# Kernel optimization log

Hardware: AMD Instinct MI355X
Metric: run time of the kernel (lower is better)

## Reference

```python
import jax, jax.numpy as jnp
import numpy as np


def setup_inputs() -> dict:
    key = jax.random.key(0)
    kq, kk, kv = jax.random.split(key, 3)
    B, S, H, D = 1, 4096, 16, 64
    q = jax.random.normal(kq, (B, S, H, D), dtype=jnp.float32)
    k = jax.random.normal(kk, (B, S, H, D), dtype=jnp.float32)
    v = jax.random.normal(kv, (B, S, H, D), dtype=jnp.float32)
    return {"q": q, "k": k, "v": v, "causal": 1}


def reference(q, k, v, causal):
    B, S, H, D = q.shape
    scale = D ** (-0.5)
    # scores: [B, H, S_q, S_k]
    scores = jnp.einsum("bqhd,bkhd->bhqk", q, k) * scale
    if causal:
        mask = jnp.triu(jnp.ones((S, S), dtype=bool), k=1)  # True above diagonal
        scores = jnp.where(mask, -jnp.inf, scores)
    attn = jax.nn.softmax(scores, axis=-1)
    out = jnp.einsum("bhqk,bkhd->bqhd", attn, v)
    return out
```

## Files before the change

kernel.cpp:

```cpp
#include <hip/hip_runtime.h>
#include <stdint.h>

#define S_LEN 4096
#define NH    16
#define HD    64
#define RSTR  (NH * HD)
#define LRSTR 18

typedef __attribute__((ext_vector_type(8))) __bf16 bf16x8;
typedef __attribute__((ext_vector_type(4))) short short4v;
typedef __attribute__((ext_vector_type(4))) float floatx4;

union BF8 { unsigned short u[8]; unsigned d[4]; uint4 q; bf16x8 v; };
union BF4 { unsigned short u[4]; unsigned d[2]; short4v s; };

__device__ __forceinline__ unsigned pkbf(float a, float b) {
    unsigned ua = __builtin_bit_cast(unsigned, a) + 0x8000u;
    unsigned ub = __builtin_bit_cast(unsigned, b) + 0x8000u;
    return __builtin_amdgcn_perm(ub, ua, 0x07060302u);
}

__device__ __forceinline__ floatx4 mfma16(short4v a, short4v b, floatx4 c) {
#if __has_builtin(__builtin_amdgcn_mfma_f32_16x16x16bf16_1k)
    return __builtin_amdgcn_mfma_f32_16x16x16bf16_1k(a, b, c, 0, 0, 0);
#else
    floatx4 d;
    asm volatile("v_mfma_f32_16x16x16_bf16 %0, %1, %2, %3\n\ts_nop 7\n\ts_nop 7"
                 : "=v"(d) : "v"(a), "v"(b), "v"(c));
    return d;
#endif
}

__device__ __forceinline__ void gl16(const void* g, void* l) {
#if __has_builtin(__builtin_amdgcn_global_load_lds)
    __builtin_amdgcn_global_load_lds((const __attribute__((address_space(1))) unsigned int*)g,
                                     (__attribute__((address_space(3))) unsigned int*)l, 16, 0, 0);
#else
    *(uint4*)l = *(const uint4*)g;
#endif
}

__global__ __launch_bounds__(256)
void pp_kv(const float* __restrict__ K, const float* __restrict__ V,
           unsigned short* __restrict__ Kz, unsigned short* __restrict__ Vz) {
    const int bid = blockIdx.x;
    const int h   = bid & 15;
    const int tau = bid >> 4;
    const int tid = threadIdx.x;
    {
        const int r = tid >> 2, gg = tid & 3;
        const float* kp = K + ((size_t)(64 * tau + r) * NH + h) * HD + 16 * gg;
        const float4 a = *reinterpret_cast<const float4*>(kp);
        const float4 b = *reinterpret_cast<const float4*>(kp + 4);
        const float4 c = *reinterpret_cast<const float4*>(kp + 8);
        const float4 d = *reinterpret_cast<const float4*>(kp + 12);
        uint4 f0, f1;
        f0.x = pkbf(a.x, a.y); f0.y = pkbf(a.z, a.w);
        f0.z = pkbf(b.x, b.y); f0.w = pkbf(b.z, b.w);
        f1.x = pkbf(c.x, c.y); f1.y = pkbf(c.z, c.w);
        f1.z = pkbf(d.x, d.y); f1.w = pkbf(d.z, d.w);
        unsigned short* out = Kz + ((size_t)(h * 64 + tau)) * 4096 + r * 64;
        *reinterpret_cast<uint4*>(out + (((2 * gg)     ^ (r & 7)) * 8)) = f0;
        *reinterpret_cast<uint4*>(out + (((2 * gg + 1) ^ (r & 7)) * 8)) = f1;
    }
    {
        const int dr = tid & 63, kg = tid >> 6;
        const float* vp = V + ((size_t)(64 * tau + 16 * kg) * NH + h) * HD + dr;
        float x[16];
        #pragma unroll
        for (int j = 0; j < 16; ++j) x[j] = vp[(size_t)j * RSTR];
        uint4 g0, g1;
        g0.x = pkbf(x[0],  x[1]);  g0.y = pkbf(x[2],  x[3]);
        g0.z = pkbf(x[4],  x[5]);  g0.w = pkbf(x[6],  x[7]);
        g1.x = pkbf(x[8],  x[9]);  g1.y = pkbf(x[10], x[11]);
        g1.z = pkbf(x[12], x[13]); g1.w = pkbf(x[14], x[15]);
        unsigned short* out = Vz + ((size_t)(h * 64 + tau)) * 4096 + dr * 64;
        *reinterpret_cast<uint4*>(out + (((2 * kg)     ^ (dr & 7)) * 8)) = g0;
        *reinterpret_cast<uint4*>(out + (((2 * kg + 1) ^ (dr & 7)) * 8)) = g1;
    }
}

__global__ __launch_bounds__(256, 4)
void fa_main(const float* __restrict__ Q, const unsigned short* __restrict__ Kz,
             const unsigned short* __restrict__ Vz, const int* __restrict__ causal_p,
             float* __restrict__ O) {
    __shared__ __align__(16) unsigned char smem[40960];
    unsigned short* Klds = (unsigned short*)smem;
    unsigned short* Vlds = (unsigned short*)(smem + 16384);
    unsigned short* Qlds = (unsigned short*)(smem + 32768);
    float* Lsum = (float*)smem;
    float* Lred = (float*)(smem + 16384);

    const int bid = blockIdx.x;
    const int h   = bid & 15;
    const int s   = bid >> 4;
    const int jj  = s & 15;
    const int kk  = s >> 4;
    int x;
    if (kk == 0) x = jj; else if (kk == 1) x = 31 - jj;
    else if (kk == 2) x = 32 + jj; else x = 63 - jj;
    const int q0 = x * 64;

    const int tid = threadIdx.x;
    const int wv  = tid >> 6;
    const int ln  = tid & 63;
    const int c16 = ln & 15;
    const int qd  = ln >> 4;
    const int causal = causal_p[0];

    const float SC = 0.18033688011112042f;

    {
        const int r = tid >> 2, gg = tid & 3;
        const float* qp = Q + ((size_t)(q0 + r) * NH + h) * HD + 16 * gg;
        const float4 a = *reinterpret_cast<const float4*>(qp);
        const float4 b = *reinterpret_cast<const float4*>(qp + 4);
        const float4 c = *reinterpret_cast<const float4*>(qp + 8);
        const float4 d = *reinterpret_cast<const float4*>(qp + 12);
        uint4 f0, f1;
        f0.x = pkbf(a.x * SC, a.y * SC); f0.y = pkbf(a.z * SC, a.w * SC);
        f0.z = pkbf(b.x * SC, b.y * SC); f0.w = pkbf(b.z * SC, b.w * SC);
        f1.x = pkbf(c.x * SC, c.y * SC); f1.y = pkbf(c.z * SC, c.w * SC);
        f1.z = pkbf(d.x * SC, d.y * SC); f1.w = pkbf(d.z * SC, d.w * SC);
        unsigned short* out = Qlds + r * 64;
        *reinterpret_cast<uint4*>(out + (((2 * gg)     ^ (r & 7)) * 8)) = f0;
        *reinterpret_cast<uint4*>(out + (((2 * gg + 1) ^ (r & 7)) * 8)) = f1;
    }

    const char* kg = (const char*)Kz + (size_t)h * 64 * 8192 + wv * 2048 + ln * 16;
    const char* vg = (const char*)Vz + (size_t)h * 64 * 8192 + wv * 2048 + ln * 16;
    char* kl = (char*)smem + wv * 2048 + ln * 16;
    char* vl = (char*)smem + 16384 + wv * 2048 + ln * 16;

#define GLDS_TILE(IT, BUF) do {                                  \
    const char* ks_ = kg + (size_t)(IT) * 8192;                  \
    const char* vs_ = vg + (size_t)(IT) * 8192;                  \
    char* kd_ = kl + (BUF) * 8192;                               \
    char* vd_ = vl + (BUF) * 8192;                               \
    gl16(ks_, kd_); gl16(ks_ + 1024, kd_ + 1024);                \
    gl16(vs_, vd_); gl16(vs_ + 1024, vd_ + 1024);                \
} while (0)

    const int nIter = causal ? (x + 1) : (S_LEN / 64);

    floatx4 acc[4][4];
    #pragma unroll
    for (int m = 0; m < 4; ++m)
        #pragma unroll
        for (int t = 0; t < 4; ++t) acc[m][t] = floatx4{0.f, 0.f, 0.f, 0.f};
    float lacc[4] = {0.f, 0.f, 0.f, 0.f};

    const int e7 = c16 & 7;
    const int o0 = (qd ^ e7) * 8;
    const int o1 = ((4 + qd) ^ e7) * 8;
    const int vo = ((2 * wv + (qd >> 1)) ^ e7) * 8 + (qd & 1) * 4;
    const int mlhs = 16 * wv + 4 * qd;

    GLDS_TILE(0, 0);
    __syncthreads();

    int cur = 0;
    for (int it = 0; it < nIter; ++it) {
        if (it + 1 < nIter) GLDS_TILE(it + 1, cur ^ 1);

        const unsigned short* Kb = Klds + cur * 4096;
        const unsigned short* Vb = Vlds + cur * 4096;

        const unsigned short* krow = Kb + (16 * wv + c16) * 64;
        const bf16x8 kf0 = *reinterpret_cast<const bf16x8*>(krow + o0);
        const bf16x8 kf1 = *reinterpret_cast<const bf16x8*>(krow + o1);

        const bool maskit = (causal != 0) && (it == nIter - 1);

        BF4 pf[4];
        #pragma unroll
        for (int t = 0; t < 4; ++t) {
            const unsigned short* qrow = Qlds + (16 * t + c16) * 64;
            const bf16x8 qf0 = *reinterpret_cast<const bf16x8*>(qrow + o0);
            const bf16x8 qf1 = *reinterpret_cast<const bf16x8*>(qrow + o1);
            floatx4 st = __builtin_amdgcn_mfma_f32_16x16x32_bf16(
                kf0, qf0, floatx4{0.f, 0.f, 0.f, 0.f}, 0, 0, 0);
            st = __builtin_amdgcn_mfma_f32_16x16x32_bf16(kf1, qf1, st, 0, 0, 0);
            float p[4];
            #pragma unroll
            for (int i = 0; i < 4; ++i) {
                float sv = st[i];
                if (maskit && (mlhs + i > 16 * t + c16)) sv = -1e30f;
                p[i] = __builtin_amdgcn_exp2f(sv);
            }
            lacc[t] += (p[0] + p[1]) + (p[2] + p[3]);
            pf[t].d[0] = pkbf(p[0], p[1]);
            pf[t].d[1] = pkbf(p[2], p[3]);
        }

        #pragma unroll
        for (int md = 0; md < 4; ++md) {
            BF4 vf;
            const unsigned short* vrow = Vb + (16 * md + c16) * 64 + vo;
            *reinterpret_cast<uint2*>(&vf.d[0]) = *reinterpret_cast<const uint2*>(vrow);
            #pragma unroll
            for (int t = 0; t < 4; ++t)
                acc[md][t] = mfma16(vf.s, pf[t].s, acc[md][t]);
        }

        __syncthreads();
        cur ^= 1;
    }

    #pragma unroll
    for (int t = 0; t < 4; ++t) {
        float lt = lacc[t];
        lt += __shfl_xor(lt, 16);
        lt += __shfl_xor(lt, 32);
        if (qd == 0) Lsum[wv * 64 + t * 16 + c16] = lt;
    }

    const int qi  = tid & 63;
    const int dg  = tid >> 6;
    const int lnr = 16 * dg + (qi & 15);
    const int jb  = 4 * (qi >> 4);
    float* orow = O + ((size_t)(q0 + qi) * NH + h) * HD;
    float inv = 0.f;

    for (int md = 0; md < 4; ++md) {
        float* Lw = Lred + (wv * 64 + ln) * LRSTR;
        #pragma unroll
        for (int t = 0; t < 4; ++t) {
            float2 w0; w0.x = acc[md][t][0]; w0.y = acc[md][t][1];
            float2 w1; w1.x = acc[md][t][2]; w1.y = acc[md][t][3];
            *reinterpret_cast<float2*>(&Lw[4 * t])     = w0;
            *reinterpret_cast<float2*>(&Lw[4 * t + 2]) = w1;
        }
        __syncthreads();
        if (md == 0) {
            const float l = Lsum[qi] + Lsum[64 + qi] + Lsum[128 + qi] + Lsum[192 + qi];
            inv = 1.0f / l;
        }
        float s0 = 0.f, s1 = 0.f, s2 = 0.f, s3 = 0.f;
        #pragma unroll
        for (int w = 0; w < 4; ++w) {
            const float* Lr = Lred + (w * 64 + lnr) * LRSTR + jb;
            s0 += Lr[0]; s1 += Lr[1]; s2 += Lr[2]; s3 += Lr[3];
        }
        floatx4 o; o[0] = s0 * inv; o[1] = s1 * inv; o[2] = s2 * inv; o[3] = s3 * inv;
        *reinterpret_cast<floatx4*>(orow + 16 * md + 4 * dg) = o;
        __syncthreads();
    }
}

extern "C" void kernel_launch(void* const* d_in, const int* in_sizes, int n_in,
                              void* d_out, int out_size, void* d_ws, size_t ws_size,
                              hipStream_t stream) {
    const float* q = (const float*)d_in[0];
    const float* k = (const float*)d_in[1];
    const float* v = (const float*)d_in[2];
    const int* causal = (const int*)d_in[3];
    float* out = (float*)d_out;
    unsigned short* Kz = (unsigned short*)d_ws;
    unsigned short* Vz = Kz + (size_t)NH * 64 * 4096;
    pp_kv<<<dim3(64 * NH), dim3(256), 0, stream>>>(k, v, Kz, Vz);
    fa_main<<<dim3(64 * NH), dim3(256), 0, stream>>>(q, Kz, Vz, causal, out);
}
```

Baseline: 160.1 us.

## Pair complementary 32-row query blocks per workgroup for causal load balance

Each workgroup now handles two 32-row query blocks, y and 127-y, instead of one 64-row block. Under the causal mask this gives every workgroup about the same number of KV tiles, replacing the earlier block-order permutation trick. Warps skip their 16-key slices when those keys lie entirely above the diagonal, and masking is applied only where keys and queries overlap. The cost is extra KV tile loads, since both phases stream keys from the start, smaller per-tile MFMA work, and a more complex two-phase epilogue with more barriers.

```diff
diff --git a/kernel.cpp b/kernel.cpp
--- a/kernel.cpp
+++ b/kernel.cpp
@@ -5,7 +5,6 @@
 #define NH    16
 #define HD    64
 #define RSTR  (NH * HD)
-#define LRSTR 18
 
 typedef __attribute__((ext_vector_type(8))) __bf16 bf16x8;
 typedef __attribute__((ext_vector_type(4))) short short4v;
@@ -89,17 +88,15 @@
     unsigned short* Vlds = (unsigned short*)(smem + 16384);
     unsigned short* Qlds = (unsigned short*)(smem + 32768);
     float* Lsum = (float*)smem;
-    float* Lred = (float*)(smem + 16384);
+    float* Lred = (float*)(smem + 1024);
 
     const int bid = blockIdx.x;
     const int h   = bid & 15;
-    const int s   = bid >> 4;
-    const int jj  = s & 15;
-    const int kk  = s >> 4;
-    int x;
-    if (kk == 0) x = jj; else if (kk == 1) x = 31 - jj;
-    else if (kk == 2) x = 32 + jj; else x = 63 - jj;
-    const int q0 = x * 64;
+    const int pr  = bid >> 4;
+    const int yA  = pr;
+    const int yB  = 127 - pr;
+    const int qbA = 32 * yA;
+    const int qbB = 32 * yB;
 
     const int tid = threadIdx.x;
     const int wv  = tid >> 6;
@@ -111,8 +108,11 @@
     const float SC = 0.18033688011112042f;
 
     {
-        const int r = tid >> 2, gg = tid & 3;
-        const float* qp = Q + ((size_t)(q0 + r) * NH + h) * HD + 16 * gg;
+        const int tl = tid >> 7;
+        const int r  = (tid >> 2) & 31;
+        const int gg = tid & 3;
+        const int qb = tl ? qbB : qbA;
+        const float* qp = Q + ((size_t)(qb + r) * NH + h) * HD + 16 * gg;
         const float4 a = *reinterpret_cast<const float4*>(qp);
         const float4 b = *reinterpret_cast<const float4*>(qp + 4);
         const float4 c = *reinterpret_cast<const float4*>(qp + 8);
@@ -122,7 +122,7 @@
         f0.z = pkbf(b.x * SC, b.y * SC); f0.w = pkbf(b.z * SC, b.w * SC);
         f1.x = pkbf(c.x * SC, c.y * SC); f1.y = pkbf(c.z * SC, c.w * SC);
         f1.z = pkbf(d.x * SC, d.y * SC); f1.w = pkbf(d.z * SC, d.w * SC);
-        unsigned short* out = Qlds + r * 64;
+        unsigned short* out = Qlds + tl * 2048 + r * 64;
         *reinterpret_cast<uint4*>(out + (((2 * gg)     ^ (r & 7)) * 8)) = f0;
         *reinterpret_cast<uint4*>(out + (((2 * gg + 1) ^ (r & 7)) * 8)) = f1;
     }
@@ -132,16 +132,18 @@
     char* kl = (char*)smem + wv * 2048 + ln * 16;
     char* vl = (char*)smem + 16384 + wv * 2048 + ln * 16;
 
-#define GLDS_TILE(IT, BUF) do {                                  \
-    const char* ks_ = kg + (size_t)(IT) * 8192;                  \
-    const char* vs_ = vg + (size_t)(IT) * 8192;                  \
+#define GLDS_TILE(TI, BUF) do {                                  \
+    const char* ks_ = kg + (size_t)(TI) * 8192;                  \
+    const char* vs_ = vg + (size_t)(TI) * 8192;                  \
     char* kd_ = kl + (BUF) * 8192;                               \
     char* vd_ = vl + (BUF) * 8192;                               \
     gl16(ks_, kd_); gl16(ks_ + 1024, kd_ + 1024);                \
     gl16(vs_, vd_); gl16(vs_ + 1024, vd_ + 1024);                \
 } while (0)
 
-    const int nIter = causal ? (x + 1) : (S_LEN / 64);
+    const int NyA = causal ? ((yA >> 1) + 1) : (S_LEN / 64);
+    const int NyB = causal ? ((yB >> 1) + 1) : (S_LEN / 64);
+    const int G   = NyA + NyB;
 
     floatx4 acc[4][4];
     #pragma unroll
@@ -154,97 +156,113 @@
     const int o0 = (qd ^ e7) * 8;
     const int o1 = ((4 + qd) ^ e7) * 8;
     const int vo = ((2 * wv + (qd >> 1)) ^ e7) * 8 + (qd & 1) * 4;
-    const int mlhs = 16 * wv + 4 * qd;
+
+#define ITER(PH, ITL) do {                                                      \
+    const int qb_ = (PH) ? qbB : qbA;                                           \
+    const unsigned short* Qb_ = Qlds + (PH) * 2048;                             \
+    const unsigned short* Kb_ = Klds + cur * 4096;                              \
+    const unsigned short* Vb_ = Vlds + cur * 4096;                              \
+    const int kvw_ = 64 * (ITL) + 16 * wv;                                      \
+    const bool skip_ = causal && (kvw_ > qb_ + 31);                             \
+    if (!skip_) {                                                               \
+        const bool needmask_ = causal && (kvw_ + 15 > qb_);                     \
+        const unsigned short* krow_ = Kb_ + (16 * wv + c16) * 64;               \
+        const bf16x8 kf0_ = *(const bf16x8*)(krow_ + o0);                       \
+        const bf16x8 kf1_ = *(const bf16x8*)(krow_ + o1);                       \
+        BF4 pf_[2];                                                             \
+        _Pragma("unroll")                                                       \
+        for (int t = 0; t < 2; ++t) {                                           \
+            const unsigned short* qrow_ = Qb_ + (16 * t + c16) * 64;            \
+            const bf16x8 qf0_ = *(const bf16x8*)(qrow_ + o0);                   \
+            const bf16x8 qf1_ = *(const bf16x8*)(qrow_ + o1);                   \
+            floatx4 st_ = __builtin_amdgcn_mfma_f32_16x16x32_bf16(              \
+                kf0_, qf0_, floatx4{0.f, 0.f, 0.f, 0.f}, 0, 0, 0);              \
+            st_ = __builtin_amdgcn_mfma_f32_16x16x32_bf16(kf1_, qf1_, st_, 0, 0, 0); \
+            const int D_ = qb_ + 16 * t + c16 - kvw_ - 4 * qd;                  \
+            float p_[4];                                                        \
+            _Pragma("unroll")                                                   \
+            for (int i = 0; i < 4; ++i) {                                       \
+                float sv_ = st_[i];                                             \
+                if (needmask_ && i > D_) sv_ = -1e30f;                          \
+                p_[i] = __builtin_amdgcn_exp2f(sv_);                            \
+            }                                                                   \
+            lacc[2 * (PH) + t] += (p_[0] + p_[1]) + (p_[2] + p_[3]);            \
+            pf_[t].d[0] = pkbf(p_[0], p_[1]);                                   \
+            pf_[t].d[1] = pkbf(p_[2], p_[3]);                                   \
+        }                                                                       \
+        _Pragma("unroll")                                                       \
+        for (int md = 0; md < 4; ++md) {                                        \
+            BF4 vf_;                                                            \
+            const unsigned short* vrow_ = Vb_ + (16 * md + c16) * 64 + vo;      \
+            *(uint2*)&vf_.d[0] = *(const uint2*)vrow_;                          \
+            acc[md][2 * (PH) + 0] = mfma16(vf_.s, pf_[0].s, acc[md][2 * (PH) + 0]); \
+            acc[md][2 * (PH) + 1] = mfma16(vf_.s, pf_[1].s, acc[md][2 * (PH) + 1]); \
+        }                                                                       \
+    }                                                                           \
+} while (0)
 
     GLDS_TILE(0, 0);
     __syncthreads();
 
     int cur = 0;
-    for (int it = 0; it < nIter; ++it) {
-        if (it + 1 < nIter) GLDS_TILE(it + 1, cur ^ 1);
-
-        const unsigned short* Kb = Klds + cur * 4096;
-        const unsigned short* Vb = Vlds + cur * 4096;
-
-        const unsigned short* krow = Kb + (16 * wv + c16) * 64;
-        const bf16x8 kf0 = *reinterpret_cast<const bf16x8*>(krow + o0);
-        const bf16x8 kf1 = *reinterpret_cast<const bf16x8*>(krow + o1);
-
-        const bool maskit = (causal != 0) && (it == nIter - 1);
-
-        BF4 pf[4];
-        #pragma unroll
-        for (int t = 0; t < 4; ++t) {
-            const unsigned short* qrow = Qlds + (16 * t + c16) * 64;
-            const bf16x8 qf0 = *reinterpret_cast<const bf16x8*>(qrow + o0);
-            const bf16x8 qf1 = *reinterpret_cast<const bf16x8*>(qrow + o1);
-            floatx4 st = __builtin_amdgcn_mfma_f32_16x16x32_bf16(
-                kf0, qf0, floatx4{0.f, 0.f, 0.f, 0.f}, 0, 0, 0);
-            st = __builtin_amdgcn_mfma_f32_16x16x32_bf16(kf1, qf1, st, 0, 0, 0);
-            float p[4];
-            #pragma unroll
-            for (int i = 0; i < 4; ++i) {
-                float sv = st[i];
-                if (maskit && (mlhs + i > 16 * t + c16)) sv = -1e30f;
-                p[i] = __builtin_amdgcn_exp2f(sv);
-            }
-            lacc[t] += (p[0] + p[1]) + (p[2] + p[3]);
-            pf[t].d[0] = pkbf(p[0], p[1]);
-            pf[t].d[1] = pkbf(p[2], p[3]);
-        }
-
-        #pragma unroll
-        for (int md = 0; md < 4; ++md) {
-            BF4 vf;
-            const unsigned short* vrow = Vb + (16 * md + c16) * 64 + vo;
-            *reinterpret_cast<uint2*>(&vf.d[0]) = *reinterpret_cast<const uint2*>(vrow);
-            #pragma unroll
-            for (int t = 0; t < 4; ++t)
-                acc[md][t] = mfma16(vf.s, pf[t].s, acc[md][t]);
-        }
-
+    for (int g = 0; g < G; ++g) {
+        const int gn = g + 1;
+        if (gn < G) GLDS_TILE(gn < NyA ? gn : gn - NyA, cur ^ 1);
+        if (g < NyA) ITER(0, g); else ITER(1, g - NyA);
         __syncthreads();
         cur ^= 1;
     }
 
+    const int qi   = tid & 31;
+    const int dg   = tid >> 5;
+    const int qdp  = dg & 3;
+    const int mds  = dg >> 2;
+    const int lnr  = 16 * qdp + (qi & 15);
+    const int tsel = qi >> 4;
+    float inv = 0.f;
+
+    float* Lw = Lred + (wv * 64 + ln) * 18 + 2 * ((ln >> 4) & 1);
+    const int rstag = 2 * ((lnr >> 4) & 1);
+
     #pragma unroll
-    for (int t = 0; t < 4; ++t) {
-        float lt = lacc[t];
-        lt += __shfl_xor(lt, 16);
-        lt += __shfl_xor(lt, 32);
-        if (qd == 0) Lsum[wv * 64 + t * 16 + c16] = lt;
-    }
-
-    const int qi  = tid & 63;
-    const int dg  = tid >> 6;
-    const int lnr = 16 * dg + (qi & 15);
-    const int jb  = 4 * (qi >> 4);
-    float* orow = O + ((size_t)(q0 + qi) * NH + h) * HD;
-    float inv = 0.f;
-
-    for (int md = 0; md < 4; ++md) {
-        float* Lw = Lred + (wv * 64 + ln) * LRSTR;
-        #pragma unroll
-        for (int t = 0; t < 4; ++t) {
-            float2 w0; w0.x = acc[md][t][0]; w0.y = acc[md][t][1];
-            float2 w1; w1.x = acc[md][t][2]; w1.y = acc[md][t][3];
-            *reinterpret_cast<float2*>(&Lw[4 * t])     = w0;
-            *reinterpret_cast<float2*>(&Lw[4 * t + 2]) = w1;
+    for (int ph = 0; ph < 2; ++ph) {
+        const int qb = ph ? qbB : qbA;
+        #pragma unroll
+        for (int t = 0; t < 2; ++t) {
+            float lt = lacc[2 * ph + t];
+            lt += __shfl_xor(lt, 16);
+            lt += __shfl_xor(lt, 32);
+            if (qd == 0) Lsum[wv * 32 + 16 * t + c16] = lt;
         }
-        __syncthreads();
-        if (md == 0) {
-            const float l = Lsum[qi] + Lsum[64 + qi] + Lsum[128 + qi] + Lsum[192 + qi];
-            inv = 1.0f / l;
+        #pragma unroll
+        for (int rd = 0; rd < 2; ++rd) {
+            #pragma unroll
+            for (int mh = 0; mh < 2; ++mh) {
+                const int md = 2 * rd + mh;
+                #pragma unroll
+                for (int t = 0; t < 2; ++t) {
+                    float2 w0; w0.x = acc[md][2 * ph + t][0]; w0.y = acc[md][2 * ph + t][1];
+                    float2 w1; w1.x = acc[md][2 * ph + t][2]; w1.y = acc[md][2 * ph + t][3];
+                    *reinterpret_cast<float2*>(&Lw[mh * 8 + t * 4])     = w0;
+                    *reinterpret_cast<float2*>(&Lw[mh * 8 + t * 4 + 2]) = w1;
+                }
+            }
+            __syncthreads();
+            if (rd == 0) {
+                const float l = Lsum[qi] + Lsum[32 + qi] + Lsum[64 + qi] + Lsum[96 + qi];
+                inv = 1.0f / l;
+            }
+            const int md = 2 * rd + mds;
+            float s0 = 0.f, s1 = 0.f, s2 = 0.f, s3 = 0.f;
+            #pragma unroll
+            for (int w = 0; w < 4; ++w) {
+                const float* Lr = Lred + (w * 64 + lnr) * 18 + rstag + mds * 8 + tsel * 4;
+                s0 += Lr[0]; s1 += Lr[1]; s2 += Lr[2]; s3 += Lr[3];
+            }
+            floatx4 o; o[0] = s0 * inv; o[1] = s1 * inv; o[2] = s2 * inv; o[3] = s3 * inv;
+            *reinterpret_cast<floatx4*>(O + ((size_t)(qb + qi) * NH + h) * HD + 16 * md + 4 * qdp) = o;
+            __syncthreads();
         }
-        float s0 = 0.f, s1 = 0.f, s2 = 0.f, s3 = 0.f;
-        #pragma unroll
-        for (int w = 0; w < 4; ++w) {
-            const float* Lr = Lred + (w * 64 + lnr) * LRSTR + jb;
-            s0 += Lr[0]; s1 += Lr[1]; s2 += Lr[2]; s3 += Lr[3];
-        }
-        floatx4 o; o[0] = s0 * inv; o[1] = s1 * inv; o[2] = s2 * inv; o[3] = s3 * inv;
-        *reinterpret_cast<floatx4*>(orow + 16 * md + 4 * dg) = o;
-        __syncthreads();
     }
 }
 
```

Result: slower. 176.9 us (+10.5%).

## Keep Q fragments in registers and compute row sums with MFMA

Applied to the files above, without the earlier changes.

Q is now loaded straight from global memory into per-lane bf16 MFMA fragments held in registers for the whole loop. This removes the Q LDS staging buffer and the per-iteration LDS reads of Q, and shrinks shared memory from 40KB to 32KB. The softmax denominator is now accumulated with an extra 16x16x16 MFMA against a ones vector, replacing the VALU adds and the cross-lane shuffle reduction. The cost is more registers for the Q fragments and the sum accumulators, plus four extra MFMAs per iteration.

```diff
diff --git a/kernel.cpp b/kernel.cpp
--- a/kernel.cpp
+++ b/kernel.cpp
@@ -5,7 +5,6 @@
 #define NH    16
 #define HD    64
 #define RSTR  (NH * HD)
-#define LRSTR 18
 
 typedef __attribute__((ext_vector_type(8))) __bf16 bf16x8;
 typedef __attribute__((ext_vector_type(4))) short short4v;
@@ -84,12 +83,11 @@
 void fa_main(const float* __restrict__ Q, const unsigned short* __restrict__ Kz,
              const unsigned short* __restrict__ Vz, const int* __restrict__ causal_p,
              float* __restrict__ O) {
-    __shared__ __align__(16) unsigned char smem[40960];
+    __shared__ __align__(16) unsigned char smem[32768];
     unsigned short* Klds = (unsigned short*)smem;
     unsigned short* Vlds = (unsigned short*)(smem + 16384);
-    unsigned short* Qlds = (unsigned short*)(smem + 32768);
     float* Lsum = (float*)smem;
-    float* Lred = (float*)(smem + 16384);
+    float* Lred = (float*)(smem + 1024);
 
     const int bid = blockIdx.x;
     const int h   = bid & 15;
@@ -110,37 +108,45 @@
 
     const float SC = 0.18033688011112042f;
 
-    {
-        const int r = tid >> 2, gg = tid & 3;
-        const float* qp = Q + ((size_t)(q0 + r) * NH + h) * HD + 16 * gg;
-        const float4 a = *reinterpret_cast<const float4*>(qp);
-        const float4 b = *reinterpret_cast<const float4*>(qp + 4);
-        const float4 c = *reinterpret_cast<const float4*>(qp + 8);
-        const float4 d = *reinterpret_cast<const float4*>(qp + 12);
-        uint4 f0, f1;
-        f0.x = pkbf(a.x * SC, a.y * SC); f0.y = pkbf(a.z * SC, a.w * SC);
-        f0.z = pkbf(b.x * SC, b.y * SC); f0.w = pkbf(b.z * SC, b.w * SC);
-        f1.x = pkbf(c.x * SC, c.y * SC); f1.y = pkbf(c.z * SC, c.w * SC);
-        f1.z = pkbf(d.x * SC, d.y * SC); f1.w = pkbf(d.z * SC, d.w * SC);
-        unsigned short* out = Qlds + r * 64;
-        *reinterpret_cast<uint4*>(out + (((2 * gg)     ^ (r & 7)) * 8)) = f0;
-        *reinterpret_cast<uint4*>(out + (((2 * gg + 1) ^ (r & 7)) * 8)) = f1;
-    }
+    const int e7 = c16 & 7;
+    const int o0 = (qd ^ e7) * 8;
+    const int o1 = ((4 + qd) ^ e7) * 8;
+    const int vo = ((2 * wv + (qd >> 1)) ^ e7) * 8 + (qd & 1) * 4;
 
     const char* kg = (const char*)Kz + (size_t)h * 64 * 8192 + wv * 2048 + ln * 16;
     const char* vg = (const char*)Vz + (size_t)h * 64 * 8192 + wv * 2048 + ln * 16;
     char* kl = (char*)smem + wv * 2048 + ln * 16;
     char* vl = (char*)smem + 16384 + wv * 2048 + ln * 16;
 
-#define GLDS_TILE(IT, BUF) do {                                  \
-    const char* ks_ = kg + (size_t)(IT) * 8192;                  \
-    const char* vs_ = vg + (size_t)(IT) * 8192;                  \
+#define GLDS_TILE(TI, BUF) do {                                  \
+    const char* ks_ = kg + (size_t)(TI) * 8192;                  \
+    const char* vs_ = vg + (size_t)(TI) * 8192;                  \
     char* kd_ = kl + (BUF) * 8192;                               \
     char* vd_ = vl + (BUF) * 8192;                               \
     gl16(ks_, kd_); gl16(ks_ + 1024, kd_ + 1024);                \
     gl16(vs_, vd_); gl16(vs_ + 1024, vd_ + 1024);                \
 } while (0)
 
+    GLDS_TILE(0, 0);
+
+    BF8 qf[4][2];
+    #pragma unroll
+    for (int t = 0; t < 4; ++t) {
+        const float* qp = Q + ((size_t)(q0 + 16 * t + c16) * NH + h) * HD + 8 * qd;
+        #pragma unroll
+        for (int c = 0; c < 2; ++c) {
+            const float4 a = *reinterpret_cast<const float4*>(qp + 32 * c);
+            const float4 b = *reinterpret_cast<const float4*>(qp + 32 * c + 4);
+            qf[t][c].d[0] = pkbf(a.x * SC, a.y * SC);
+            qf[t][c].d[1] = pkbf(a.z * SC, a.w * SC);
+            qf[t][c].d[2] = pkbf(b.x * SC, b.y * SC);
+            qf[t][c].d[3] = pkbf(b.z * SC, b.w * SC);
+        }
+    }
+
+    BF4 ones;
+    ones.d[0] = 0x3F803F80u; ones.d[1] = 0x3F803F80u;
+
     const int nIter = causal ? (x + 1) : (S_LEN / 64);
 
     floatx4 acc[4][4];
@@ -148,15 +154,10 @@
     for (int m = 0; m < 4; ++m)
         #pragma unroll
         for (int t = 0; t < 4; ++t) acc[m][t] = floatx4{0.f, 0.f, 0.f, 0.f};
-    float lacc[4] = {0.f, 0.f, 0.f, 0.f};
-
-    const int e7 = c16 & 7;
-    const int o0 = (qd ^ e7) * 8;
-    const int o1 = ((4 + qd) ^ e7) * 8;
-    const int vo = ((2 * wv + (qd >> 1)) ^ e7) * 8 + (qd & 1) * 4;
-    const int mlhs = 16 * wv + 4 * qd;
-
-    GLDS_TILE(0, 0);
+    floatx4 lcc[4];
+    #pragma unroll
+    for (int t = 0; t < 4; ++t) lcc[t] = floatx4{0.f, 0.f, 0.f, 0.f};
+
     __syncthreads();
 
     int cur = 0;
@@ -175,22 +176,20 @@
         BF4 pf[4];
         #pragma unroll
         for (int t = 0; t < 4; ++t) {
-            const unsigned short* qrow = Qlds + (16 * t + c16) * 64;
-            const bf16x8 qf0 = *reinterpret_cast<const bf16x8*>(qrow + o0);
-            const bf16x8 qf1 = *reinterpret_cast<const bf16x8*>(qrow + o1);
             floatx4 st = __builtin_amdgcn_mfma_f32_16x16x32_bf16(
-                kf0, qf0, floatx4{0.f, 0.f, 0.f, 0.f}, 0, 0, 0);
-            st = __builtin_amdgcn_mfma_f32_16x16x32_bf16(kf1, qf1, st, 0, 0, 0);
+                kf0, qf[t][0].v, floatx4{0.f, 0.f, 0.f, 0.f}, 0, 0, 0);
+            st = __builtin_amdgcn_mfma_f32_16x16x32_bf16(kf1, qf[t][1].v, st, 0, 0, 0);
+            const int D = 16 * t + c16 - 16 * wv - 4 * qd;
             float p[4];
             #pragma unroll
             for (int i = 0; i < 4; ++i) {
                 float sv = st[i];
-                if (maskit && (mlhs + i > 16 * t + c16)) sv = -1e30f;
+                if (maskit && (i > D)) sv = -1e30f;
                 p[i] = __builtin_amdgcn_exp2f(sv);
             }
-            lacc[t] += (p[0] + p[1]) + (p[2] + p[3]);
             pf[t].d[0] = pkbf(p[0], p[1]);
             pf[t].d[1] = pkbf(p[2], p[3]);
+            lcc[t] = mfma16(ones.s, pf[t].s, lcc[t]);
         }
 
         #pragma unroll
@@ -208,12 +207,8 @@
     }
 
     #pragma unroll
-    for (int t = 0; t < 4; ++t) {
-        float lt = lacc[t];
-        lt += __shfl_xor(lt, 16);
-        lt += __shfl_xor(lt, 32);
-        if (qd == 0) Lsum[wv * 64 + t * 16 + c16] = lt;
-    }
+    for (int t = 0; t < 4; ++t)
+        if (qd == 0) Lsum[wv * 64 + t * 16 + c16] = lcc[t][0];
 
     const int qi  = tid & 63;
     const int dg  = tid >> 6;
@@ -223,7 +218,7 @@
     float inv = 0.f;
 
     for (int md = 0; md < 4; ++md) {
-        float* Lw = Lred + (wv * 64 + ln) * LRSTR;
+        float* Lw = Lred + (wv * 64 + ln) * 18;
         #pragma unroll
         for (int t = 0; t < 4; ++t) {
             float2 w0; w0.x = acc[md][t][0]; w0.y = acc[md][t][1];
@@ -239,7 +234,7 @@
         float s0 = 0.f, s1 = 0.f, s2 = 0.f, s3 = 0.f;
         #pragma unroll
         for (int w = 0; w < 4; ++w) {
-            const float* Lr = Lred + (w * 64 + lnr) * LRSTR + jb;
+            const float* Lr = Lred + (w * 64 + lnr) * 18 + jb;
             s0 += Lr[0]; s1 += Lr[1]; s2 += Lr[2]; s3 += Lr[3];
         }
         floatx4 o; o[0] = s0 * inv; o[1] = s1 * inv; o[2] = s2 * inv; o[3] = s3 * inv;
```

Measured after the change: 205.4 us. +28.3%, slower.
